# Kernel optimization log

Measured on AMD Instinct MI355X. Metric: run time of the kernel, lower is better.

The kernel has to match this reference:

```python
import jax, jax.numpy as jnp
import numpy as np

B = 16      # number of point clouds
N = 4096    # points per cloud (max after densify)
D = 3       # xyz


def setup_inputs() -> dict:
    key = jax.random.key(0)
    k1, k2 = jax.random.split(key)
    pred = jax.random.normal(k1, (B * N, D), dtype=jnp.float32)
    target = jax.random.normal(k2, (B * N, D), dtype=jnp.float32)
    # sorted segment ids, equal-sized clouds (faithful to to_dense_batch usage)
    batch = jnp.repeat(jnp.arange(B, dtype=jnp.int64), N)
    return {"pred": pred, "target": target, "batch": batch}


def to_dense_batch(x, batch, num_batches, max_n):
    # PyG to_dense_batch: scatter flat points into [B, max_n, D], zero-padded.
    ones = jnp.ones_like(batch)
    counts = jax.ops.segment_sum(ones, batch, num_segments=num_batches)
    offsets = jnp.concatenate([jnp.zeros((1,), batch.dtype), jnp.cumsum(counts)[:-1]])
    pos = jnp.arange(batch.shape[0], dtype=batch.dtype) - offsets[batch]
    dense = jnp.zeros((num_batches, max_n, x.shape[-1]), x.dtype)
    return dense.at[batch, pos].set(x)


def chamfer_distance(x, y):
    # squared-euclidean pairwise distances via the GEMM identity
    x2 = jnp.sum(x * x, axis=-1)                      # [B, N]
    y2 = jnp.sum(y * y, axis=-1)                      # [B, M]
    xy = jnp.einsum('bnd,bmd->bnm', x, y)             # [B, N, M]
    d = x2[:, :, None] + y2[:, None, :] - 2.0 * xy    # [B, N, M]
    cham_x = jnp.mean(jnp.min(d, axis=2), axis=1)     # mean over N of min over M
    cham_y = jnp.mean(jnp.min(d, axis=1), axis=1)     # mean over M of min over N
    # point_reduction='mean', batch_reduction='mean' (pytorch3d defaults)
    return jnp.mean(cham_x + cham_y)


def reference(pred, target, batch):
    x = to_dense_batch(pred, batch, B, N)
    y = to_dense_batch(target, batch, B, N)
    return chamfer_distance(x, y)
```

## Files before the change

kernel.cpp:

```cpp
#include <hip/hip_runtime.h>


namespace {

constexpr int kB = 16;
constexpr int kN = 4096;
constexpr int kNTH = 256;
constexpr int kTILE = 256;
constexpr int kPlane = kB * kN;
constexpr float kScale = 1.0f / (float)(kB * kN);

__global__ void init_out(float* out) { out[0] = 0.0f; }

template <int KX, int S, bool DIRECT>
__global__ __launch_bounds__(kNTH) void chamfer_min(
    const float* __restrict__ pred, const float* __restrict__ targ,
    float* __restrict__ part, float* __restrict__ out) {
  __shared__ float4 ytile[kTILE];

  const int t = threadIdx.x;
  const int xb = blockIdx.x;
  const int b = blockIdx.y;
  const int z = blockIdx.z;
  const int dir = z / S;
  const int slice = z % S;

  if constexpr (!DIRECT) {
    if (t == 0) out[0] = 0.0f;
  }

  const float* __restrict__ X = dir ? targ : pred;
  const float* __restrict__ Y = dir ? pred : targ;

  float xpx[KX], xpy[KX], xpz[KX], x2[KX], mn[KX];
  const int ibase = b * kN + xb * (kNTH * KX) + t;
#pragma unroll
  for (int k = 0; k < KX; ++k) {
    const int i = ibase + k * kNTH;
    const float a = X[3 * i], c = X[3 * i + 1], d = X[3 * i + 2];
    x2[k] = fmaf(a, a, fmaf(c, c, d * d));
    xpx[k] = -2.0f * a; xpy[k] = -2.0f * c; xpz[k] = -2.0f * d;
    mn[k] = 1e30f;
  }

  constexpr int YSL = kN / S;
  const int ybase = b * kN + slice * YSL;
  for (int t0 = 0; t0 < YSL; t0 += kTILE) {
    const int j = ybase + t0 + t;
    const float a = Y[3 * j], c = Y[3 * j + 1], d = Y[3 * j + 2];
    __syncthreads();
    ytile[t] = make_float4(a, c, d, fmaf(a, a, fmaf(c, c, d * d)));
    __syncthreads();
#pragma unroll 4
    for (int jj = 0; jj < kTILE; jj += 2) {
      const float4 q0 = ytile[jj];
      const float4 q1 = ytile[jj + 1];
#pragma unroll
      for (int k = 0; k < KX; ++k) {
        const float v0 =
            fmaf(xpx[k], q0.x, fmaf(xpy[k], q0.y, fmaf(xpz[k], q0.z, q0.w)));
        const float v1 =
            fmaf(xpx[k], q1.x, fmaf(xpy[k], q1.y, fmaf(xpz[k], q1.z, q1.w)));
        mn[k] = fminf(mn[k], fminf(v0, v1));
      }
    }
  }

  if constexpr (DIRECT) {
    float s = 0.0f;
#pragma unroll
    for (int k = 0; k < KX; ++k) s += x2[k] + mn[k];
    for (int o = 32; o > 0; o >>= 1) s += __shfl_down(s, o, 64);
    __shared__ float wsum[kNTH / 64];
    const int lane = t & 63, w = t >> 6;
    if (lane == 0) wsum[w] = s;
    __syncthreads();
    if (t == 0) {
      float tot = 0.0f;
#pragma unroll
      for (int w2 = 0; w2 < kNTH / 64; ++w2) tot += wsum[w2];
      atomicAdd(out, tot * kScale);
    }
  } else {
#pragma unroll
    for (int k = 0; k < KX; ++k)
      part[(size_t)z * kPlane + (ibase + k * kNTH)] = x2[k] + mn[k];
  }
}

template <int S, int RQ>
__global__ __launch_bounds__(256) void chamfer_reduce(
    const float* __restrict__ part, float* __restrict__ out) {
  float s = 0.0f;
#pragma unroll
  for (int r = 0; r < RQ; ++r) {
    const int u = blockIdx.x * (256 * RQ) + r * 256 + threadIdx.x;
    const int dir = u >> 16;
    const int q = u & (kPlane - 1);
    float m = 1e30f;
#pragma unroll
    for (int sl = 0; sl < S; ++sl)
      m = fminf(m, part[(size_t)(dir * S + sl) * kPlane + q]);
    s += m;
  }
  for (int o = 32; o > 0; o >>= 1) s += __shfl_down(s, o, 64);
  __shared__ float wsum[4];
  const int lane = threadIdx.x & 63, w = threadIdx.x >> 6;
  if (lane == 0) wsum[w] = s;
  __syncthreads();
  if (threadIdx.x == 0)
    atomicAdd(out, (wsum[0] + wsum[1] + wsum[2] + wsum[3]) * kScale);
}

}

extern "C" void kernel_launch(void* const* d_in, const int* in_sizes, int n_in,
                              void* d_out, int out_size, void* d_ws,
                              size_t ws_size, hipStream_t stream) {
  const float* pred = (const float*)d_in[0];
  const float* targ = (const float*)d_in[1];
  float* out = (float*)d_out;
  float* part = (float*)d_ws;

  constexpr int KX = 8;
  constexpr int RQ = 8;
  const size_t need16 = (size_t)2 * 16 * kPlane * sizeof(float);
  const size_t need8 = (size_t)2 * 8 * kPlane * sizeof(float);
  const size_t need4 = (size_t)2 * 4 * kPlane * sizeof(float);
  if (ws_size >= need16) {
    constexpr int S = 16;
    dim3 grid(kN / (kNTH * KX), kB, 2 * S);
    chamfer_min<KX, S, false><<<grid, kNTH, 0, stream>>>(pred, targ, part, out);
    chamfer_reduce<S, RQ>
        <<<dim3(2 * kPlane / (256 * RQ)), 256, 0, stream>>>(part, out);
  } else if (ws_size >= need8) {
    constexpr int S = 8;
    dim3 grid(kN / (kNTH * KX), kB, 2 * S);
    chamfer_min<KX, S, false><<<grid, kNTH, 0, stream>>>(pred, targ, part, out);
    chamfer_reduce<S, RQ>
        <<<dim3(2 * kPlane / (256 * RQ)), 256, 0, stream>>>(part, out);
  } else if (ws_size >= need4) {
    constexpr int S = 4;
    dim3 grid(kN / (kNTH * KX), kB, 2 * S);
    chamfer_min<KX, S, false><<<grid, kNTH, 0, stream>>>(pred, targ, part, out);
    chamfer_reduce<S, RQ>
        <<<dim3(2 * kPlane / (256 * RQ)), 256, 0, stream>>>(part, out);
  } else {
    init_out<<<dim3(1), dim3(1), 0, stream>>>(out);
    constexpr int KX2 = 2;
    dim3 grid(kN / (kNTH * KX2), kB, 2);
    chamfer_min<KX2, 1, true><<<grid, kNTH, 0, stream>>>(pred, targ, nullptr,
                                                         out);
  }
}
```

Before: 115.0 us.

## Use packed FP32 FMA with SoA pair tiles and min3 in chamfer inner loop

```diff
diff --git a/kernel.cpp b/kernel.cpp
--- a/kernel.cpp
+++ b/kernel.cpp
@@ -16,7 +16,8 @@
 __global__ __launch_bounds__(kNTH) void chamfer_min(
     const float* __restrict__ pred, const float* __restrict__ targ,
     float* __restrict__ part, float* __restrict__ out) {
-  __shared__ float4 ytile[kTILE];
+  __shared__ float4 tA[kTILE / 2];
+  __shared__ float4 tB[kTILE / 2];
 
   const int t = threadIdx.x;
   const int xb = blockIdx.x;
@@ -32,36 +33,55 @@
   const float* __restrict__ X = dir ? targ : pred;
   const float* __restrict__ Y = dir ? pred : targ;
 
-  float xpx[KX], xpy[KX], xpz[KX], x2[KX], mn[KX];
+  float2 xx2[KX], xy2[KX], xz2[KX];
+  float x2[KX], mn[KX];
   const int ibase = b * kN + xb * (kNTH * KX) + t;
 #pragma unroll
   for (int k = 0; k < KX; ++k) {
     const int i = ibase + k * kNTH;
     const float a = X[3 * i], c = X[3 * i + 1], d = X[3 * i + 2];
     x2[k] = fmaf(a, a, fmaf(c, c, d * d));
-    xpx[k] = -2.0f * a; xpy[k] = -2.0f * c; xpz[k] = -2.0f * d;
+    const float pa = -2.0f * a, pc = -2.0f * c, pd = -2.0f * d;
+    xx2[k] = make_float2(pa, pa);
+    xy2[k] = make_float2(pc, pc);
+    xz2[k] = make_float2(pd, pd);
     mn[k] = 1e30f;
   }
 
   constexpr int YSL = kN / S;
   const int ybase = b * kN + slice * YSL;
   for (int t0 = 0; t0 < YSL; t0 += kTILE) {
-    const int j = ybase + t0 + t;
-    const float a = Y[3 * j], c = Y[3 * j + 1], d = Y[3 * j + 2];
     __syncthreads();
-    ytile[t] = make_float4(a, c, d, fmaf(a, a, fmaf(c, c, d * d)));
+    if (t < kTILE / 2) {
+      const int j0 = 3 * (ybase + t0 + 2 * t);
+      const float a0 = Y[j0], c0 = Y[j0 + 1], d0 = Y[j0 + 2];
+      const float a1 = Y[j0 + 3], c1 = Y[j0 + 4], d1 = Y[j0 + 5];
+      tA[t] = make_float4(a0, a1, c0, c1);
+      tB[t] = make_float4(d0, d1, fmaf(a0, a0, fmaf(c0, c0, d0 * d0)),
+                          fmaf(a1, a1, fmaf(c1, c1, d1 * d1)));
+    }
     __syncthreads();
-#pragma unroll 4
-    for (int jj = 0; jj < kTILE; jj += 2) {
-      const float4 q0 = ytile[jj];
-      const float4 q1 = ytile[jj + 1];
+#pragma unroll 2
+    for (int jj = 0; jj < kTILE / 2; ++jj) {
+      const float4 qa = tA[jj];
+      const float4 qb = tB[jj];
+      const float2 qx = make_float2(qa.x, qa.y);
+      const float2 qy = make_float2(qa.z, qa.w);
+      const float2 qz = make_float2(qb.x, qb.y);
+      const float2 qw = make_float2(qb.z, qb.w);
 #pragma unroll
       for (int k = 0; k < KX; ++k) {
-        const float v0 =
-            fmaf(xpx[k], q0.x, fmaf(xpy[k], q0.y, fmaf(xpz[k], q0.z, q0.w)));
-        const float v1 =
-            fmaf(xpx[k], q1.x, fmaf(xpy[k], q1.y, fmaf(xpz[k], q1.z, q1.w)));
-        mn[k] = fminf(mn[k], fminf(v0, v1));
+        float2 acc;
+        asm("v_pk_fma_f32 %0, %1, %2, %3\n\t"
+            "v_pk_fma_f32 %0, %4, %5, %0\n\t"
+            "v_pk_fma_f32 %0, %6, %7, %0"
+            : "=&v"(acc)
+            : "v"(xz2[k]), "v"(qz), "v"(qw),
+              "v"(xy2[k]), "v"(qy),
+              "v"(xx2[k]), "v"(qx));
+        asm("v_min3_f32 %0, %0, %1, %2"
+            : "+v"(mn[k])
+            : "v"(acc.x), "v"(acc.y));
       }
     }
   }
@@ -123,7 +143,7 @@
   float* part = (float*)d_ws;
 
   constexpr int KX = 8;
-  constexpr int RQ = 8;
+  constexpr int RQ = 2;
   const size_t need16 = (size_t)2 * 16 * kPlane * sizeof(float);
   const size_t need8 = (size_t)2 * 8 * kPlane * sizeof(float);
   const size_t need4 = (size_t)2 * 4 * kPlane * sizeof(float);
```

Measured after the change: 101.3 us. 1.14x faster.
